# Kernel tuning notes

Hardware: AMD Instinct MI355X
Metric: run time of the kernel (lower is better)

Reference implementation:

```python
import jax, jax.numpy as jnp
import numpy as np

PI = 3.141592653589793
TINY = 1e-6
B = 1048576

DH_INIT = np.array([[0.0, 180.0, -650.0, 0.0],
                    [270.0, 90.0, 0.0, 0.0],
                    [800.0, 0.0, 0.0, 0.0],
                    [140.0, 90.0, -908.0, 0.0],
                    [0.0, -96.0, 0.0, 0.0],
                    [0.0, -65.0, 260.0, 0.0]], dtype=np.float32)


def setup_inputs() -> dict:
    key = jax.random.key(0)
    theta = jax.random.normal(key, (B, 6), dtype=jnp.float32) * 90.0  # joint angles in degrees
    dh = jnp.asarray(DH_INIT)  # trainable (6,4) DH table [a, alpha_deg, d, theta_offset_deg]
    return {"theta": theta, "dh": dh}


def _rad(x):
    return x * (PI / 180.0)


def _deg(x):
    return x * (180.0 / PI)


def _divide_no_nan(num, den):
    safe = jnp.where(den == 0.0, 1.0, den)
    return jnp.where(den == 0.0, 0.0, num / safe)


def _fk(theta, dh):
    # theta: (B,6) degrees; dh: (6,4)
    a = dh[:, 0]            # (6,)
    alpha = _rad(dh[:, 1])  # (6,)
    d = dh[:, 2]            # (6,)
    th = _rad(dh[:, 3][None, :] + theta)  # (B,6)

    ct, st = jnp.cos(th), jnp.sin(th)                    # (B,6)
    ca, sa = jnp.cos(alpha), jnp.sin(alpha)              # (6,)
    z = jnp.zeros_like(ct)
    one = jnp.ones_like(ct)
    ab = jnp.broadcast_to(a, ct.shape)
    cab = jnp.broadcast_to(ca, ct.shape)
    sab = jnp.broadcast_to(sa, ct.shape)
    sdb = jnp.broadcast_to(-sa * d, ct.shape)
    cdb = jnp.broadcast_to(ca * d, ct.shape)

    # Modified-DH joint transforms, shape (B,6,4,4)
    T = jnp.stack([
        jnp.stack([ct, -st, z, ab], axis=-1),
        jnp.stack([st * cab, ct * cab, -sab, sdb], axis=-1),
        jnp.stack([st * sab, ct * sab, cab, cdb], axis=-1),
        jnp.stack([z, z, z, one], axis=-1),
    ], axis=-2)

    # Chain the 6 transforms: b = T0 @ T1 @ ... @ T5, batched over B
    b = T[:, 0]
    for i in range(1, 6):  # fixed small structural loop over joints
        b = jnp.einsum('bij,bjk->bik', b, T[:, i])

    # Euler angle extraction (ZYX-style with gimbal-lock branch)
    T00, T01, T02 = b[:, 0, 0], b[:, 0, 1], b[:, 0, 2]
    T10, T11, T12 = b[:, 1, 0], b[:, 1, 1], b[:, 1, 2]
    T22 = b[:, 2, 2]
    cond = (jnp.abs(T12) <= TINY) & (jnp.abs(T22) <= TINY)

    # singular case (C = 0, cos(C) = 1)
    cC = jnp.float32(1.0)
    B_s = _deg(jnp.arctan2(T02, _divide_no_nan(T22, cC)))
    A_s = _deg(jnp.arctan2(T10, _divide_no_nan(T11, cC)))
    C_s = jnp.zeros_like(B_s)

    # normal case
    A_n = _deg(jnp.arctan2(-T01, T00))
    sA = jnp.sin(_rad(A_n))
    cA = jnp.cos(_rad(A_n))
    B_n = _deg(jnp.arctan2(T02, cA * T00 - sA * T01))
    C_n = _deg(jnp.arctan2(-T12, T22))

    A = jnp.where(cond, A_s, A_n)
    Bd = jnp.where(cond, B_s, B_n)
    C = jnp.where(cond, C_s, C_n)

    return jnp.stack([b[:, 0, 3], b[:, 1, 3], b[:, 2, 3], A, Bd, C], axis=-1)  # (B,6)


def reference(theta, dh):
    return _fk(theta, dh)
```

## Files before the change

### kernel.cpp

```cpp
#include <hip/hip_runtime.h>
#include <math.h>


#define PI_D   3.141592653589793
#define RAD_D  (PI_D / 180.0)
#define RAD_F  0.017453292519943295f
#define DEG_F  57.29577951308232f
#define TINY_D 1e-6

__device__ __forceinline__ void sincos_deg(double xdeg, double* s, double* c)
{
    const double qf = rint(xdeg * (1.0 / 90.0));
    const double r  = fma(qf, -90.0, xdeg) * RAD_D;
    const int q = ((int)qf) & 3;
    const double z = r * r;

    double sp = 1.58962301576546568060e-10;
    sp = fma(sp, z, -2.50507477628578072866e-8);
    sp = fma(sp, z,  2.75573136213857245213e-6);
    sp = fma(sp, z, -1.98412698295895385996e-4);
    sp = fma(sp, z,  8.33333333332211858878e-3);
    sp = fma(sp, z, -1.66666666666666307295e-1);
    const double sr = fma(r * z, sp, r);

    double cp = -1.13585365213876817300e-11;
    cp = fma(cp, z,  2.08757008419747316778e-9);
    cp = fma(cp, z, -2.75573141792967388112e-7);
    cp = fma(cp, z,  2.48015872888517179954e-5);
    cp = fma(cp, z, -1.38888888888730564116e-3);
    cp = fma(cp, z,  4.16666666666665929218e-2);
    const double cr = fma(z * z, cp, fma(z, -0.5, 1.0));

    double ss = (q & 1) ? cr : sr;
    double cc = (q & 1) ? sr : cr;
    ss = (q & 2)       ? -ss : ss;
    cc = ((q + 1) & 2) ? -cc : cc;
    *s = ss; *c = cc;
}

__device__ __forceinline__ void sincosf_deg(float xdeg, float* s, float* c)
{
    const float qf = rintf(xdeg * (1.0f / 90.0f));
    const float r  = fmaf(qf, -90.0f, xdeg) * RAD_F;
    const int q = ((int)qf) & 3;
    const float z = r * r;

    float sp = -1.9515295891e-4f;
    sp = fmaf(sp, z,  8.3321608736e-3f);
    sp = fmaf(sp, z, -1.6666654611e-1f);
    const float sr = fmaf(r * z, sp, r);

    float cp =  2.443315711809948e-5f;
    cp = fmaf(cp, z, -1.388731625493765e-3f);
    cp = fmaf(cp, z,  4.166664568298827e-2f);
    const float cr = fmaf(z * z, cp, fmaf(z, -0.5f, 1.0f));

    float ss = (q & 1) ? cr : sr;
    float cc = (q & 1) ? sr : cr;
    ss = (q & 2)       ? -ss : ss;
    cc = ((q + 1) & 2) ? -cc : cc;
    *s = ss; *c = cc;
}

__global__ __launch_bounds__(256)
void fk6_kernel(const float* __restrict__ theta,
                const float* __restrict__ dh,
                float* __restrict__ out,
                int B)
{
    __shared__ double s_a[6], s_ca[6], s_sa[6], s_nsd[6], s_cd[6], s_th0[6];
    __shared__ float  f_a[6], f_ca[6], f_sa[6], f_nsd[6], f_cd[6], f_th0[6];
    if (threadIdx.x < 6) {
        const int i = threadIdx.x;
        const double a   = (double)dh[i * 4 + 0];
        const double alp = (double)dh[i * 4 + 1];
        const double d   = (double)dh[i * 4 + 2];
        const double th0 = (double)dh[i * 4 + 3];
        double sa, ca;
        sincos_deg(alp, &sa, &ca);
        s_a[i] = a;  s_ca[i] = ca;  s_sa[i] = sa;
        s_nsd[i] = -sa * d;  s_cd[i] = ca * d;  s_th0[i] = th0;
        f_a[i] = (float)a;  f_ca[i] = (float)ca;  f_sa[i] = (float)sa;
        f_nsd[i] = (float)(-sa * d);  f_cd[i] = (float)(ca * d);  f_th0[i] = (float)th0;
    }
    __syncthreads();

    const long long b = (long long)blockIdx.x * blockDim.x + threadIdx.x;
    if (b >= B) return;

    const float2* tp = reinterpret_cast<const float2*>(theta + 6ll * b);
    const float2 v01 = tp[0];
    const float2 v23 = tp[1];
    const float2 v45 = tp[2];
    const float thf[6] = { v01.x, v01.y, v23.x, v23.y, v45.x, v45.y };

    float st[6], ct[6];
    #pragma unroll
    for (int i = 0; i < 6; ++i)
        sincosf_deg(f_th0[i] + thf[i], &st[i], &ct[i]);

    float M[3][4];
    {
        const float ca = f_ca[0], sa = f_sa[0];
        M[0][0] = ct[0];      M[0][1] = -st[0];     M[0][2] = 0.0f; M[0][3] = f_a[0];
        M[1][0] = st[0] * ca; M[1][1] = ct[0] * ca; M[1][2] = -sa;  M[1][3] = f_nsd[0];
        M[2][0] = st[0] * sa; M[2][1] = ct[0] * sa; M[2][2] = ca;   M[2][3] = f_cd[0];
    }
    #pragma unroll
    for (int i = 1; i < 6; ++i) {
        const float ca = f_ca[i], sa = f_sa[i];
        const float t00 = ct[i],      t01 = -st[i],     t03 = f_a[i];
        const float t10 = st[i] * ca, t11 = ct[i] * ca, t12 = -sa, t13 = f_nsd[i];
        const float t20 = st[i] * sa, t21 = ct[i] * sa, t22 = ca,  t23 = f_cd[i];
        #pragma unroll
        for (int r = 0; r < 3; ++r) {
            const float m0 = M[r][0], m1 = M[r][1], m2 = M[r][2], m3 = M[r][3];
            M[r][0] = m0 * t00 + m1 * t10 + m2 * t20;
            M[r][1] = m0 * t01 + m1 * t11 + m2 * t21;
            M[r][2] =            m1 * t12 + m2 * t22;
            M[r][3] = m0 * t03 + m1 * t13 + m2 * t23 + m3;
        }
    }

    const float T00 = M[0][0], T01 = M[0][1], T02 = M[0][2];
    const float T12 = M[1][2], T22 = M[2][2];

    float ox = M[0][3], oy = M[1][3], oz = M[2][3];
    float A  = atan2f(-T01, T00) * DEG_F;
    float Bd = atan2f(T02, sqrtf(fmaf(T00, T00, T01 * T01))) * DEG_F;
    float C  = atan2f(-T12, T22) * DEG_F;

    const bool risky = (fabsf(T01) < 1e-4f) | (fabsf(T12) < 1e-4f) |
                       (fmaf(T00, T00, T01 * T01) < 1e-6f) |
                       (fmaf(T12, T12, T22 * T22) < 1e-6f);

    if (__builtin_expect(risky, 0)) {
        double dst[6], dct[6];
        #pragma unroll
        for (int i = 0; i < 6; ++i)
            sincos_deg(s_th0[i] + (double)thf[i], &dst[i], &dct[i]);

        double D[3][4];
        {
            const double ca = s_ca[0], sa = s_sa[0];
            D[0][0] = dct[0];      D[0][1] = -dst[0];     D[0][2] = 0.0; D[0][3] = s_a[0];
            D[1][0] = dst[0] * ca; D[1][1] = dct[0] * ca; D[1][2] = -sa; D[1][3] = s_nsd[0];
            D[2][0] = dst[0] * sa; D[2][1] = dct[0] * sa; D[2][2] = ca;  D[2][3] = s_cd[0];
        }
        #pragma unroll
        for (int i = 1; i < 6; ++i) {
            const double ca = s_ca[i], sa = s_sa[i];
            const double t00 = dct[i],      t01 = -dst[i],     t03 = s_a[i];
            const double t10 = dst[i] * ca, t11 = dct[i] * ca, t12 = -sa, t13 = s_nsd[i];
            const double t20 = dst[i] * sa, t21 = dct[i] * sa, t22 = ca,  t23 = s_cd[i];
            #pragma unroll
            for (int r = 0; r < 3; ++r) {
                const double m0 = D[r][0], m1 = D[r][1], m2 = D[r][2], m3 = D[r][3];
                D[r][0] = m0 * t00 + m1 * t10 + m2 * t20;
                D[r][1] = m0 * t01 + m1 * t11 + m2 * t21;
                D[r][2] =            m1 * t12 + m2 * t22;
                D[r][3] = m0 * t03 + m1 * t13 + m2 * t23 + m3;
            }
        }
        const float d00 = (float)D[0][0], d01 = (float)D[0][1], d02 = (float)D[0][2];
        const float d12 = (float)D[1][2], d22 = (float)D[2][2];

        ox = (float)D[0][3]; oy = (float)D[1][3]; oz = (float)D[2][3];
        A  = atan2f(-d01, d00) * DEG_F;
        Bd = atan2f(d02, sqrtf(fmaf(d00, d00, d01 * d01))) * DEG_F;
        C  = atan2f(-d12, d22) * DEG_F;
        if (fabs(D[1][2]) <= TINY_D && fabs(D[2][2]) <= TINY_D) {
            Bd = atan2f(d02, d22) * DEG_F;
            A  = atan2f((float)D[1][0], (float)D[1][1]) * DEG_F;
            C  = 0.0f;
        }
    }

    float2* op = reinterpret_cast<float2*>(out + 6ll * b);
    op[0] = make_float2(ox, oy);
    op[1] = make_float2(oz, A);
    op[2] = make_float2(Bd, C);
}

extern "C" void kernel_launch(void* const* d_in, const int* in_sizes, int n_in,
                              void* d_out, int out_size, void* d_ws, size_t ws_size,
                              hipStream_t stream) {
    const float* theta = (const float*)d_in[0];
    const float* dh    = (const float*)d_in[1];
    float* out = (float*)d_out;

    const int B = in_sizes[0] / 6;
    const int block = 256;
    const int grid = (B + block - 1) / block;
    fk6_kernel<<<grid, block, 0, stream>>>(theta, dh, out, B);
}
```

Before: 22.68 us.

## Split FK into a lean float kernel plus a compacted double-precision fixup pass

The single kernel is split in two. A fast kernel runs only the float path, writes every output, and atomically appends the indices of numerically risky rows to a workspace list. A second small kernel recomputes only those rows in double precision and overwrites their outputs. This removes the double-precision code and shared tables from the main kernel to cut register pressure and raise occupancy, but adds a memset, an extra launch and atomics. If the risky count exceeds the workspace capacity, the overflow rows keep their float-path values.

```diff
diff --git a/kernel.cpp b/kernel.cpp
--- a/kernel.cpp
+++ b/kernel.cpp
@@ -62,11 +62,173 @@
     *s = ss; *c = cc;
 }
 
+__global__ __launch_bounds__(256, 8)
+void fk6_fast(const float* __restrict__ theta,
+              const float* __restrict__ dh,
+              float* __restrict__ out,
+              unsigned* __restrict__ risk_cnt,
+              unsigned* __restrict__ risk_idx,
+              unsigned cap,
+              int B)
+{
+    __shared__ float f_a[6], f_ca[6], f_sa[6], f_nsd[6], f_cd[6], f_th0[6];
+    if (threadIdx.x < 6) {
+        const int i = threadIdx.x;
+        const float a   = dh[i * 4 + 0];
+        const float alp = dh[i * 4 + 1];
+        const float d   = dh[i * 4 + 2];
+        float sa, ca;
+        sincosf_deg(alp, &sa, &ca);
+        f_a[i] = a;  f_ca[i] = ca;  f_sa[i] = sa;
+        f_nsd[i] = -sa * d;  f_cd[i] = ca * d;
+        f_th0[i] = dh[i * 4 + 3];
+    }
+    __syncthreads();
+
+    const long long b = (long long)blockIdx.x * blockDim.x + threadIdx.x;
+    if (b >= B) return;
+
+    const float2* tp = reinterpret_cast<const float2*>(theta + 6ll * b);
+    const float2 v01 = tp[0];
+    const float2 v23 = tp[1];
+    const float2 v45 = tp[2];
+    const float thf[6] = { v01.x, v01.y, v23.x, v23.y, v45.x, v45.y };
+
+    float st[6], ct[6];
+    #pragma unroll
+    for (int i = 0; i < 6; ++i)
+        sincosf_deg(f_th0[i] + thf[i], &st[i], &ct[i]);
+
+    float M[3][4];
+    {
+        const float ca = f_ca[0], sa = f_sa[0];
+        M[0][0] = ct[0];      M[0][1] = -st[0];     M[0][2] = 0.0f; M[0][3] = f_a[0];
+        M[1][0] = st[0] * ca; M[1][1] = ct[0] * ca; M[1][2] = -sa;  M[1][3] = f_nsd[0];
+        M[2][0] = st[0] * sa; M[2][1] = ct[0] * sa; M[2][2] = ca;   M[2][3] = f_cd[0];
+    }
+    #pragma unroll
+    for (int i = 1; i < 6; ++i) {
+        const float ca = f_ca[i], sa = f_sa[i];
+        const float t00 = ct[i],      t01 = -st[i],     t03 = f_a[i];
+        const float t10 = st[i] * ca, t11 = ct[i] * ca, t12 = -sa, t13 = f_nsd[i];
+        const float t20 = st[i] * sa, t21 = ct[i] * sa, t22 = ca,  t23 = f_cd[i];
+        #pragma unroll
+        for (int r = 0; r < 3; ++r) {
+            const float m0 = M[r][0], m1 = M[r][1], m2 = M[r][2], m3 = M[r][3];
+            M[r][0] = m0 * t00 + m1 * t10 + m2 * t20;
+            M[r][1] = m0 * t01 + m1 * t11 + m2 * t21;
+            M[r][2] =            m1 * t12 + m2 * t22;
+            M[r][3] = m0 * t03 + m1 * t13 + m2 * t23 + m3;
+        }
+    }
+
+    const float T00 = M[0][0], T01 = M[0][1], T02 = M[0][2];
+    const float T12 = M[1][2], T22 = M[2][2];
+
+    const float A  = atan2f(-T01, T00) * DEG_F;
+    const float Bd = atan2f(T02, sqrtf(fmaf(T00, T00, T01 * T01))) * DEG_F;
+    const float C  = atan2f(-T12, T22) * DEG_F;
+
+    float2* op = reinterpret_cast<float2*>(out + 6ll * b);
+    op[0] = make_float2(M[0][3], M[1][3]);
+    op[1] = make_float2(M[2][3], A);
+    op[2] = make_float2(Bd, C);
+
+    const bool risky = (fabsf(T01) < 1e-4f) | (fabsf(T12) < 1e-4f) |
+                       (fmaf(T00, T00, T01 * T01) < 1e-6f) |
+                       (fmaf(T12, T12, T22 * T22) < 1e-6f);
+    if (__builtin_expect(risky, 0)) {
+        const unsigned idx = atomicAdd(risk_cnt, 1u);
+        if (idx < cap) risk_idx[idx] = (unsigned)b;
+    }
+}
+
+__global__ void fk6_fix(const float* __restrict__ theta,
+                        const float* __restrict__ dh,
+                        float* __restrict__ out,
+                        const unsigned* __restrict__ risk_cnt,
+                        const unsigned* __restrict__ risk_idx,
+                        unsigned cap)
+{
+    __shared__ double s_a[6], s_ca[6], s_sa[6], s_nsd[6], s_cd[6], s_th0[6];
+    if (threadIdx.x < 6) {
+        const int i = threadIdx.x;
+        const double a   = (double)dh[i * 4 + 0];
+        const double alp = (double)dh[i * 4 + 1];
+        const double d   = (double)dh[i * 4 + 2];
+        double sa, ca;
+        sincos_deg(alp, &sa, &ca);
+        s_a[i] = a;  s_ca[i] = ca;  s_sa[i] = sa;
+        s_nsd[i] = -sa * d;  s_cd[i] = ca * d;
+        s_th0[i] = (double)dh[i * 4 + 3];
+    }
+    __syncthreads();
+
+    unsigned n = *risk_cnt;
+    if (n > cap) n = cap;
+
+    for (unsigned t = blockIdx.x * blockDim.x + threadIdx.x; t < n;
+         t += gridDim.x * blockDim.x) {
+        const long long b = (long long)risk_idx[t];
+        const float2* tp = reinterpret_cast<const float2*>(theta + 6ll * b);
+        const float2 v01 = tp[0];
+        const float2 v23 = tp[1];
+        const float2 v45 = tp[2];
+        const double th[6] = { (double)v01.x, (double)v01.y,
+                               (double)v23.x, (double)v23.y,
+                               (double)v45.x, (double)v45.y };
+
+        double dst[6], dct[6];
+        #pragma unroll
+        for (int i = 0; i < 6; ++i)
+            sincos_deg(s_th0[i] + th[i], &dst[i], &dct[i]);
+
+        double D[3][4];
+        {
+            const double ca = s_ca[0], sa = s_sa[0];
+            D[0][0] = dct[0];      D[0][1] = -dst[0];     D[0][2] = 0.0; D[0][3] = s_a[0];
+            D[1][0] = dst[0] * ca; D[1][1] = dct[0] * ca; D[1][2] = -sa; D[1][3] = s_nsd[0];
+            D[2][0] = dst[0] * sa; D[2][1] = dct[0] * sa; D[2][2] = ca;  D[2][3] = s_cd[0];
+        }
+        #pragma unroll
+        for (int i = 1; i < 6; ++i) {
+            const double ca = s_ca[i], sa = s_sa[i];
+            const double t00 = dct[i],      t01 = -dst[i],     t03 = s_a[i];
+            const double t10 = dst[i] * ca, t11 = dct[i] * ca, t12 = -sa, t13 = s_nsd[i];
+            const double t20 = dst[i] * sa, t21 = dct[i] * sa, t22 = ca,  t23 = s_cd[i];
+            #pragma unroll
+            for (int r = 0; r < 3; ++r) {
+                const double m0 = D[r][0], m1 = D[r][1], m2 = D[r][2], m3 = D[r][3];
+                D[r][0] = m0 * t00 + m1 * t10 + m2 * t20;
+                D[r][1] = m0 * t01 + m1 * t11 + m2 * t21;
+                D[r][2] =            m1 * t12 + m2 * t22;
+                D[r][3] = m0 * t03 + m1 * t13 + m2 * t23 + m3;
+            }
+        }
+        const float d00 = (float)D[0][0], d01 = (float)D[0][1], d02 = (float)D[0][2];
+        const float d12 = (float)D[1][2], d22 = (float)D[2][2];
+
+        float A  = atan2f(-d01, d00) * DEG_F;
+        float Bd = atan2f(d02, sqrtf(fmaf(d00, d00, d01 * d01))) * DEG_F;
+        float C  = atan2f(-d12, d22) * DEG_F;
+        if (fabs(D[1][2]) <= TINY_D && fabs(D[2][2]) <= TINY_D) {
+            Bd = atan2f(d02, d22) * DEG_F;
+            A  = atan2f((float)D[1][0], (float)D[1][1]) * DEG_F;
+            C  = 0.0f;
+        }
+
+        float2* op = reinterpret_cast<float2*>(out + 6ll * b);
+        op[0] = make_float2((float)D[0][3], (float)D[1][3]);
+        op[1] = make_float2((float)D[2][3], A);
+        op[2] = make_float2(Bd, C);
+    }
+}
+
 __global__ __launch_bounds__(256)
-void fk6_kernel(const float* __restrict__ theta,
-                const float* __restrict__ dh,
-                float* __restrict__ out,
-                int B)
+void fk6_combined(const float* __restrict__ theta,
+                  const float* __restrict__ dh,
+                  float* __restrict__ out,
+                  int B)
 {
     __shared__ double s_a[6], s_ca[6], s_sa[6], s_nsd[6], s_cd[6], s_th0[6];
     __shared__ float  f_a[6], f_ca[6], f_sa[6], f_nsd[6], f_cd[6], f_th0[6];
@@ -192,5 +354,16 @@
     const int B = in_sizes[0] / 6;
     const int block = 256;
     const int grid = (B + block - 1) / block;
-    fk6_kernel<<<grid, block, 0, stream>>>(theta, dh, out, B);
-}
+
+    if (ws_size >= 65536) {
+        unsigned* risk_cnt = (unsigned*)d_ws;
+        unsigned* risk_idx = (unsigned*)((char*)d_ws + 256);
+        const unsigned cap = (unsigned)((ws_size - 256) / 4);
+        hipMemsetAsync(d_ws, 0, 4, stream);
+        fk6_fast<<<grid, block, 0, stream>>>(theta, dh, out,
+                                             risk_cnt, risk_idx, cap, B);
+        fk6_fix<<<16, 256, 0, stream>>>(theta, dh, out, risk_cnt, risk_idx, cap);
+    } else {
+        fk6_combined<<<grid, block, 0, stream>>>(theta, dh, out, B);
+    }
+}
```

Result: slower. 64.91 us (+186.2%).

## Process two elements per thread with float4 I/O and out-of-line fp64 fixup

Applied to the files above, without the earlier changes.

Each thread now handles two batch elements, loading and storing them with three float4 accesses instead of float2 accesses, and halves the grid. The last joint multiply computes only the matrix entries needed for the output. The fp64 fallback moves into a separate function that re-reads theta and overwrites the output only for flagged elements. This aims to widen memory transactions and add independent work per thread, at the cost of more register pressure and fewer threads.

```diff
diff --git a/kernel.cpp b/kernel.cpp
--- a/kernel.cpp
+++ b/kernel.cpp
@@ -2,11 +2,15 @@
 #include <math.h>
 
 
-#define PI_D   3.141592653589793
-#define RAD_D  (PI_D / 180.0)
+#define RAD_D  (3.141592653589793 / 180.0)
 #define RAD_F  0.017453292519943295f
 #define DEG_F  57.29577951308232f
 #define TINY_D 1e-6
+
+struct DHShared {
+    double a[6], ca[6], sa[6], nsd[6], cd[6], th0[6];
+    float  fa[6], fca[6], fsa[6], fnsd[6], fcd[6], fth0[6];
+};
 
 __device__ __forceinline__ void sincos_deg(double xdeg, double* s, double* c)
 {
@@ -62,14 +66,127 @@
     *s = ss; *c = cc;
 }
 
+__device__ __forceinline__ void fk_f32(const float* __restrict__ thf,
+                                       const DHShared& K,
+                                       float res[6], bool& risky)
+{
+    float st[6], ct[6];
+    #pragma unroll
+    for (int i = 0; i < 6; ++i)
+        sincosf_deg(K.fth0[i] + thf[i], &st[i], &ct[i]);
+
+    float M[3][4];
+    {
+        const float ca = K.fca[0], sa = K.fsa[0];
+        M[0][0] = ct[0];      M[0][1] = -st[0];     M[0][2] = 0.0f; M[0][3] = K.fa[0];
+        M[1][0] = st[0] * ca; M[1][1] = ct[0] * ca; M[1][2] = -sa;  M[1][3] = K.fnsd[0];
+        M[2][0] = st[0] * sa; M[2][1] = ct[0] * sa; M[2][2] = ca;   M[2][3] = K.fcd[0];
+    }
+    #pragma unroll
+    for (int i = 1; i < 5; ++i) {
+        const float ca = K.fca[i], sa = K.fsa[i];
+        const float t00 = ct[i],      t01 = -st[i],     t03 = K.fa[i];
+        const float t10 = st[i] * ca, t11 = ct[i] * ca, t12 = -sa, t13 = K.fnsd[i];
+        const float t20 = st[i] * sa, t21 = ct[i] * sa, t22 = ca,  t23 = K.fcd[i];
+        #pragma unroll
+        for (int r = 0; r < 3; ++r) {
+            const float m0 = M[r][0], m1 = M[r][1], m2 = M[r][2], m3 = M[r][3];
+            M[r][0] = m0 * t00 + m1 * t10 + m2 * t20;
+            M[r][1] = m0 * t01 + m1 * t11 + m2 * t21;
+            M[r][2] =            m1 * t12 + m2 * t22;
+            M[r][3] = m0 * t03 + m1 * t13 + m2 * t23 + m3;
+        }
+    }
+    {
+        const float ca = K.fca[5], sa = K.fsa[5];
+        const float t00 = ct[5],      t01 = -st[5],     t03 = K.fa[5];
+        const float t10 = st[5] * ca, t11 = ct[5] * ca, t12 = -sa, t13 = K.fnsd[5];
+        const float t20 = st[5] * sa, t21 = ct[5] * sa, t22 = ca,  t23 = K.fcd[5];
+
+        const float T00 = M[0][0]*t00 + M[0][1]*t10 + M[0][2]*t20;
+        const float T01 = M[0][0]*t01 + M[0][1]*t11 + M[0][2]*t21;
+        const float T02 =               M[0][1]*t12 + M[0][2]*t22;
+        const float x   = M[0][0]*t03 + M[0][1]*t13 + M[0][2]*t23 + M[0][3];
+        const float T12 =               M[1][1]*t12 + M[1][2]*t22;
+        const float y   = M[1][0]*t03 + M[1][1]*t13 + M[1][2]*t23 + M[1][3];
+        const float T22 =               M[2][1]*t12 + M[2][2]*t22;
+        const float z   = M[2][0]*t03 + M[2][1]*t13 + M[2][2]*t23 + M[2][3];
+
+        res[0] = x; res[1] = y; res[2] = z;
+        res[3] = atan2f(-T01, T00) * DEG_F;
+        res[4] = atan2f(T02, sqrtf(fmaf(T00, T00, T01 * T01))) * DEG_F;
+        res[5] = atan2f(-T12, T22) * DEG_F;
+
+        risky = (fabsf(T01) < 1e-4f) | (fabsf(T12) < 1e-4f) |
+                (fmaf(T00, T00, T01 * T01) < 1e-6f) |
+                (fmaf(T12, T12, T22 * T22) < 1e-6f);
+    }
+}
+
+__device__ __forceinline__ void fix_elem(const float* __restrict__ theta,
+                                         float* __restrict__ out,
+                                         const DHShared& K, long long b)
+{
+    const float2* tp = reinterpret_cast<const float2*>(theta + 6ll * b);
+    const float2 v01 = tp[0];
+    const float2 v23 = tp[1];
+    const float2 v45 = tp[2];
+    const double th[6] = { (double)v01.x, (double)v01.y,
+                           (double)v23.x, (double)v23.y,
+                           (double)v45.x, (double)v45.y };
+
+    double dst[6], dct[6];
+    #pragma unroll
+    for (int i = 0; i < 6; ++i)
+        sincos_deg(K.th0[i] + th[i], &dst[i], &dct[i]);
+
+    double D[3][4];
+    {
+        const double ca = K.ca[0], sa = K.sa[0];
+        D[0][0] = dct[0];      D[0][1] = -dst[0];     D[0][2] = 0.0; D[0][3] = K.a[0];
+        D[1][0] = dst[0] * ca; D[1][1] = dct[0] * ca; D[1][2] = -sa; D[1][3] = K.nsd[0];
+        D[2][0] = dst[0] * sa; D[2][1] = dct[0] * sa; D[2][2] = ca;  D[2][3] = K.cd[0];
+    }
+    #pragma unroll
+    for (int i = 1; i < 6; ++i) {
+        const double ca = K.ca[i], sa = K.sa[i];
+        const double t00 = dct[i],      t01 = -dst[i],     t03 = K.a[i];
+        const double t10 = dst[i] * ca, t11 = dct[i] * ca, t12 = -sa, t13 = K.nsd[i];
+        const double t20 = dst[i] * sa, t21 = dct[i] * sa, t22 = ca,  t23 = K.cd[i];
+        #pragma unroll
+        for (int r = 0; r < 3; ++r) {
+            const double m0 = D[r][0], m1 = D[r][1], m2 = D[r][2], m3 = D[r][3];
+            D[r][0] = m0 * t00 + m1 * t10 + m2 * t20;
+            D[r][1] = m0 * t01 + m1 * t11 + m2 * t21;
+            D[r][2] =            m1 * t12 + m2 * t22;
+            D[r][3] = m0 * t03 + m1 * t13 + m2 * t23 + m3;
+        }
+    }
+    const float d00 = (float)D[0][0], d01 = (float)D[0][1], d02 = (float)D[0][2];
+    const float d12 = (float)D[1][2], d22 = (float)D[2][2];
+
+    float A  = atan2f(-d01, d00) * DEG_F;
+    float Bd = atan2f(d02, sqrtf(fmaf(d00, d00, d01 * d01))) * DEG_F;
+    float C  = atan2f(-d12, d22) * DEG_F;
+    if (fabs(D[1][2]) <= TINY_D && fabs(D[2][2]) <= TINY_D) {
+        Bd = atan2f(d02, d22) * DEG_F;
+        A  = atan2f((float)D[1][0], (float)D[1][1]) * DEG_F;
+        C  = 0.0f;
+    }
+
+    float2* op = reinterpret_cast<float2*>(out + 6ll * b);
+    op[0] = make_float2((float)D[0][3], (float)D[1][3]);
+    op[1] = make_float2((float)D[2][3], A);
+    op[2] = make_float2(Bd, C);
+}
+
 __global__ __launch_bounds__(256)
-void fk6_kernel(const float* __restrict__ theta,
-                const float* __restrict__ dh,
-                float* __restrict__ out,
-                int B)
-{
-    __shared__ double s_a[6], s_ca[6], s_sa[6], s_nsd[6], s_cd[6], s_th0[6];
-    __shared__ float  f_a[6], f_ca[6], f_sa[6], f_nsd[6], f_cd[6], f_th0[6];
+void fk6_x2(const float* __restrict__ theta,
+            const float* __restrict__ dh,
+            float* __restrict__ out,
+            int B)
+{
+    __shared__ DHShared K;
     if (threadIdx.x < 6) {
         const int i = threadIdx.x;
         const double a   = (double)dh[i * 4 + 0];
@@ -78,108 +195,54 @@
         const double th0 = (double)dh[i * 4 + 3];
         double sa, ca;
         sincos_deg(alp, &sa, &ca);
-        s_a[i] = a;  s_ca[i] = ca;  s_sa[i] = sa;
-        s_nsd[i] = -sa * d;  s_cd[i] = ca * d;  s_th0[i] = th0;
-        f_a[i] = (float)a;  f_ca[i] = (float)ca;  f_sa[i] = (float)sa;
-        f_nsd[i] = (float)(-sa * d);  f_cd[i] = (float)(ca * d);  f_th0[i] = (float)th0;
+        K.a[i] = a;  K.ca[i] = ca;  K.sa[i] = sa;
+        K.nsd[i] = -sa * d;  K.cd[i] = ca * d;  K.th0[i] = th0;
+        K.fa[i]   = (float)a;        K.fca[i] = (float)ca;  K.fsa[i] = (float)sa;
+        K.fnsd[i] = (float)(-sa*d);  K.fcd[i] = (float)(ca*d);
+        K.fth0[i] = (float)th0;
     }
     __syncthreads();
 
-    const long long b = (long long)blockIdx.x * blockDim.x + threadIdx.x;
-    if (b >= B) return;
-
-    const float2* tp = reinterpret_cast<const float2*>(theta + 6ll * b);
-    const float2 v01 = tp[0];
-    const float2 v23 = tp[1];
-    const float2 v45 = tp[2];
-    const float thf[6] = { v01.x, v01.y, v23.x, v23.y, v45.x, v45.y };
-
-    float st[6], ct[6];
-    #pragma unroll
-    for (int i = 0; i < 6; ++i)
-        sincosf_deg(f_th0[i] + thf[i], &st[i], &ct[i]);
-
-    float M[3][4];
-    {
-        const float ca = f_ca[0], sa = f_sa[0];
-        M[0][0] = ct[0];      M[0][1] = -st[0];     M[0][2] = 0.0f; M[0][3] = f_a[0];
-        M[1][0] = st[0] * ca; M[1][1] = ct[0] * ca; M[1][2] = -sa;  M[1][3] = f_nsd[0];
-        M[2][0] = st[0] * sa; M[2][1] = ct[0] * sa; M[2][2] = ca;   M[2][3] = f_cd[0];
-    }
-    #pragma unroll
-    for (int i = 1; i < 6; ++i) {
-        const float ca = f_ca[i], sa = f_sa[i];
-        const float t00 = ct[i],      t01 = -st[i],     t03 = f_a[i];
-        const float t10 = st[i] * ca, t11 = ct[i] * ca, t12 = -sa, t13 = f_nsd[i];
-        const float t20 = st[i] * sa, t21 = ct[i] * sa, t22 = ca,  t23 = f_cd[i];
-        #pragma unroll
-        for (int r = 0; r < 3; ++r) {
-            const float m0 = M[r][0], m1 = M[r][1], m2 = M[r][2], m3 = M[r][3];
-            M[r][0] = m0 * t00 + m1 * t10 + m2 * t20;
-            M[r][1] = m0 * t01 + m1 * t11 + m2 * t21;
-            M[r][2] =            m1 * t12 + m2 * t22;
-            M[r][3] = m0 * t03 + m1 * t13 + m2 * t23 + m3;
-        }
-    }
-
-    const float T00 = M[0][0], T01 = M[0][1], T02 = M[0][2];
-    const float T12 = M[1][2], T22 = M[2][2];
-
-    float ox = M[0][3], oy = M[1][3], oz = M[2][3];
-    float A  = atan2f(-T01, T00) * DEG_F;
-    float Bd = atan2f(T02, sqrtf(fmaf(T00, T00, T01 * T01))) * DEG_F;
-    float C  = atan2f(-T12, T22) * DEG_F;
-
-    const bool risky = (fabsf(T01) < 1e-4f) | (fabsf(T12) < 1e-4f) |
-                       (fmaf(T00, T00, T01 * T01) < 1e-6f) |
-                       (fmaf(T12, T12, T22 * T22) < 1e-6f);
-
-    if (__builtin_expect(risky, 0)) {
-        double dst[6], dct[6];
-        #pragma unroll
-        for (int i = 0; i < 6; ++i)
-            sincos_deg(s_th0[i] + (double)thf[i], &dst[i], &dct[i]);
-
-        double D[3][4];
-        {
-            const double ca = s_ca[0], sa = s_sa[0];
-            D[0][0] = dct[0];      D[0][1] = -dst[0];     D[0][2] = 0.0; D[0][3] = s_a[0];
-            D[1][0] = dst[0] * ca; D[1][1] = dct[0] * ca; D[1][2] = -sa; D[1][3] = s_nsd[0];
-            D[2][0] = dst[0] * sa; D[2][1] = dct[0] * sa; D[2][2] = ca;  D[2][3] = s_cd[0];
-        }
-        #pragma unroll
-        for (int i = 1; i < 6; ++i) {
-            const double ca = s_ca[i], sa = s_sa[i];
-            const double t00 = dct[i],      t01 = -dst[i],     t03 = s_a[i];
-            const double t10 = dst[i] * ca, t11 = dct[i] * ca, t12 = -sa, t13 = s_nsd[i];
-            const double t20 = dst[i] * sa, t21 = dct[i] * sa, t22 = ca,  t23 = s_cd[i];
-            #pragma unroll
-            for (int r = 0; r < 3; ++r) {
-                const double m0 = D[r][0], m1 = D[r][1], m2 = D[r][2], m3 = D[r][3];
-                D[r][0] = m0 * t00 + m1 * t10 + m2 * t20;
-                D[r][1] = m0 * t01 + m1 * t11 + m2 * t21;
-                D[r][2] =            m1 * t12 + m2 * t22;
-                D[r][3] = m0 * t03 + m1 * t13 + m2 * t23 + m3;
+    const long long t  = (long long)blockIdx.x * blockDim.x + threadIdx.x;
+    const long long b0 = 2 * t;
+    const long long b1 = 2 * t + 1;
+    if (b0 >= B) return;
+
+    if (__builtin_expect(b1 < B, 1)) {
+        const float4* tp = reinterpret_cast<const float4*>(theta + 12ll * t);
+        const float4 u0 = tp[0], u1 = tp[1], u2 = tp[2];
+        const float th0f[6] = { u0.x, u0.y, u0.z, u0.w, u1.x, u1.y };
+        const float th1f[6] = { u1.z, u1.w, u2.x, u2.y, u2.z, u2.w };
+
+        float r0[6], r1[6];
+        bool k0, k1;
+        fk_f32(th0f, K, r0, k0);
+        fk_f32(th1f, K, r1, k1);
+
+        float4* op = reinterpret_cast<float4*>(out + 12ll * t);
+        op[0] = make_float4(r0[0], r0[1], r0[2], r0[3]);
+        op[1] = make_float4(r0[4], r0[5], r1[0], r1[1]);
+        op[2] = make_float4(r1[2], r1[3], r1[4], r1[5]);
+
+        if (__builtin_expect(k0 | k1, 0)) {
+            #pragma unroll 1
+            for (int e = 0; e < 2; ++e) {
+                const bool k = e ? k1 : k0;
+                if (k) fix_elem(theta, out, K, b0 + e);
             }
         }
-        const float d00 = (float)D[0][0], d01 = (float)D[0][1], d02 = (float)D[0][2];
-        const float d12 = (float)D[1][2], d22 = (float)D[2][2];
-
-        ox = (float)D[0][3]; oy = (float)D[1][3]; oz = (float)D[2][3];
-        A  = atan2f(-d01, d00) * DEG_F;
-        Bd = atan2f(d02, sqrtf(fmaf(d00, d00, d01 * d01))) * DEG_F;
-        C  = atan2f(-d12, d22) * DEG_F;
-        if (fabs(D[1][2]) <= TINY_D && fabs(D[2][2]) <= TINY_D) {
-            Bd = atan2f(d02, d22) * DEG_F;
-            A  = atan2f((float)D[1][0], (float)D[1][1]) * DEG_F;
-            C  = 0.0f;
-        }
-    }
-
-    float2* op = reinterpret_cast<float2*>(out + 6ll * b);
-    op[0] = make_float2(ox, oy);
-    op[1] = make_float2(oz, A);
-    op[2] = make_float2(Bd, C);
+    } else {
+        const float2* tp = reinterpret_cast<const float2*>(theta + 6ll * b0);
+        const float2 v01 = tp[0], v23 = tp[1], v45 = tp[2];
+        const float thf[6] = { v01.x, v01.y, v23.x, v23.y, v45.x, v45.y };
+        float r[6]; bool k;
+        fk_f32(thf, K, r, k);
+        float2* op = reinterpret_cast<float2*>(out + 6ll * b0);
+        op[0] = make_float2(r[0], r[1]);
+        op[1] = make_float2(r[2], r[3]);
+        op[2] = make_float2(r[4], r[5]);
+        if (k) fix_elem(theta, out, K, b0);
+    }
 }
 
 extern "C" void kernel_launch(void* const* d_in, const int* in_sizes, int n_in,
@@ -191,6 +254,7 @@
 
     const int B = in_sizes[0] / 6;
     const int block = 256;
-    const int grid = (B + block - 1) / block;
-    fk6_kernel<<<grid, block, 0, stream>>>(theta, dh, out, B);
-}
+    const long long pairs = ((long long)B + 1) / 2;
+    const int grid = (int)((pairs + block - 1) / block);
+    fk6_x2<<<grid, block, 0, stream>>>(theta, dh, out, B);
+}
```

New measurement: 25.58 us. 12.8% more time.
